# Optimization experiments

Hardware: AMD Instinct MI355X
Metric: run time of the kernel (lower is better)

The kernel has to match this reference:

```python
import jax, jax.numpy as jnp
import numpy as np

MEAN_STOP_TIME_S = 60.0
MIN_ROUTE_LEN = 2
DEMAND_TIME_WEIGHT = 0.5
ROUTE_TIME_WEIGHT = 0.5
UNSERVED_WEIGHT = 5.0

B, N, R, L, K = 64, 512, 40, 20, 4


def setup_inputs() -> dict:
    key = jax.random.key(0)
    ks = jax.random.split(key, 8)
    demand = jax.random.uniform(ks[0], (B, N, N), dtype=jnp.float32) * 10.0
    drive_times = jax.random.uniform(ks[1], (B, N, N), dtype=jnp.float32) * 1800.0
    transit_times = jax.random.uniform(ks[2], (B, N, N), dtype=jnp.float32) * 3600.0
    has_path = jax.random.randint(ks[3], (B, N, N), 0, 2) > 0
    n_transfers = jax.random.randint(ks[4], (B, N, N), 0, 4).astype(jnp.int32)
    # routes with -1 padding past a random per-route length
    routes = jax.random.randint(ks[5], (B, R, L), 0, N).astype(jnp.int32)
    lens = jax.random.randint(ks[6], (B, R), 0, L + 1)
    valid = jnp.arange(L)[None, None, :] < lens[:, :, None]
    batch_routes = jnp.where(valid, routes, -1)
    # per demand-edge route assignments, -1 = unused slot
    route_seqs = (jax.random.randint(ks[7], (B, N, N, K), 0, R + 1) - 1).astype(jnp.int32)
    return {
        'demand': demand, 'drive_times': drive_times, 'transit_times': transit_times,
        'has_path': has_path, 'n_transfers': n_transfers,
        'batch_routes': batch_routes, 'route_seqs': route_seqs,
    }


def _route_leg_times(batch_routes, dtm, mean_stop_time_s):
    # leg (l -> l+1) of each route: dtm[b, from, to] + stop time, masked on valid stops
    frm = batch_routes[:, :, :-1]
    to = batch_routes[:, :, 1:]
    valid = (frm >= 0) & (to >= 0)
    bidx = jnp.arange(dtm.shape[0])[:, None, None]
    times = dtm[bidx, jnp.maximum(frm, 0), jnp.maximum(to, 0)] + mean_stop_time_s
    return jnp.where(valid, times, 0.0)  # [B, R, L-1]


def _per_route_riders(demand, route_seqs, n_routes):
    # segment-sum demand over route ids; -1 slots go to a dump bucket
    def per_b(dem, rs):
        ids = rs.reshape(-1)
        vals = jnp.broadcast_to(dem[..., None], rs.shape).reshape(-1)
        ids = jnp.where(ids < 0, n_routes, ids)
        return jax.ops.segment_sum(vals, ids, num_segments=n_routes + 1)[:n_routes]
    return jax.vmap(per_b)(demand, route_seqs)  # [B, R]


def reference(demand, drive_times, transit_times, has_path, n_transfers,
              batch_routes, route_seqs):
    fdem = demand
    nopath = ~has_path
    route_lens = (batch_routes > -1).sum(-1)  # [B, R]

    n_disconnected = (nopath & (fdem > 0)).sum(axis=(1, 2))
    route_len_delta = jnp.maximum(MIN_ROUTE_LEN - route_lens, 0)
    route_len_delta = jnp.where(route_lens == 0, 0, route_len_delta)
    n_stops_oob = route_len_delta.sum(-1)  # [B]

    nt_eff = jnp.where(nopath, 3, n_transfers)
    tat = jnp.stack([
        (fdem * (nt_eff == 0)).sum(axis=(1, 2)),
        (fdem * (nt_eff == 1)).sum(axis=(1, 2)),
        (fdem * (nt_eff == 2)).sum(axis=(1, 2)),
        (fdem * (nt_eff > 2)).sum(axis=(1, 2)),
    ], axis=-1)  # trips_at_transfers [B, 4]

    trip_times = jnp.where(nopath, 0.0, transit_times)
    total_dmd_time = (fdem * trip_times).sum(axis=(1, 2))
    total_transfers = (fdem * n_transfers.astype(fdem.dtype)).sum(axis=(1, 2))
    unserved = (fdem * nopath).sum(axis=(1, 2))
    total_demand = fdem.sum(axis=(1, 2))

    leg_times = _route_leg_times(batch_routes, drive_times, MEAN_STOP_TIME_S)
    total_route_time = leg_times.sum(axis=(1, 2))
    # symmetric_routes=True: add return-direction legs
    ret = _route_leg_times(batch_routes, jnp.swapaxes(drive_times, 1, 2), MEAN_STOP_TIME_S)
    total_route_time = total_route_time + ret.sum(axis=(1, 2))

    per_route_riders = _per_route_riders(fdem, route_seqs, R)

    # cost assembly
    time_norm = drive_times.max(axis=(1, 2))
    served = total_demand - unserved
    mean_dmd_time = total_dmd_time / (served + 1e-6)
    norm_dmd_time = mean_dmd_time / time_norm
    n_routes_used = (route_lens > 0).sum(-1)
    norm_route_time = total_route_time / (time_norm * n_routes_used + 1e-6)
    n_demand_edges = (fdem > 0).sum(axis=(1, 2))
    frac_uncovered = n_disconnected / n_demand_edges
    denom = n_routes_used * MIN_ROUTE_LEN
    frac_oob = n_stops_oob / (denom + 1e-6)
    cost = (DEMAND_TIME_WEIGHT * norm_dmd_time
            + ROUTE_TIME_WEIGHT * norm_route_time
            + UNSERVED_WEIGHT * (frac_uncovered + frac_oob))
    return cost, per_route_riders, tat, total_route_time


if __name__ == '__main__':
    out = reference(**setup_inputs())
    print([o.shape for o in out])
```

## Files before the change

### kernel.cpp

```cpp
#include <hip/hip_runtime.h>

#define NB 64
#define NDIM 512
#define NNE (NDIM * NDIM)
#define NR 40
#define NL 20
#define SUBS 16
#define IT 16

#define MAIN_STRIDE 256
#define FLAG_OFF (NB * SUBS * MAIN_STRIDE)
#define OUT_RIDERS 64
#define OUT_TAT (64 + NB * NR)
#define OUT_TRT (64 + NB * NR + NB * 4)

__global__ void detect_kernel(const unsigned int* __restrict__ hp, int* __restrict__ flag) {
    unsigned int v = hp[threadIdx.x];
    unsigned long long m = __ballot(v > 1u);
    if (threadIdx.x == 0) *flag = (m != 0ull) ? 1 : 0;
}

struct G {
    float4 dem, tt, dt;
    int4 nt, r0, r1, r2, r3;
    int h0, h1, h2, h3;
};

template<bool BYTE>
__device__ __forceinline__ void ld(G& g,
    const float* __restrict__ pd, const float* __restrict__ pt,
    const float* __restrict__ pdr, const int* __restrict__ pn,
    const void* __restrict__ ph, const int* __restrict__ pr, int o)
{
    g.dem = *(const float4*)(pd + o);
    g.tt  = *(const float4*)(pt + o);
    g.dt  = *(const float4*)(pdr + o);
    g.nt  = *(const int4*)(pn + o);
    g.r0  = *(const int4*)(pr + o * 4);
    g.r1  = *(const int4*)(pr + o * 4 + 4);
    g.r2  = *(const int4*)(pr + o * 4 + 8);
    g.r3  = *(const int4*)(pr + o * 4 + 12);
    if (BYTE) {
        const uchar4 hb = *(const uchar4*)((const unsigned char*)ph + o);
        g.h0 = hb.x; g.h1 = hb.y; g.h2 = hb.z; g.h3 = hb.w;
    } else {
        const int4 hw = *(const int4*)((const int*)ph + o);
        g.h0 = hw.x; g.h1 = hw.y; g.h2 = hw.z; g.h3 = hw.w;
    }
}

__device__ __forceinline__ void procE(float d, float ttv, float dtv, int ntv, int hv,
                                      int i0, int i1, int i2, int i3,
                                      float acc[10], float* __restrict__ bcol)
{
    const bool np_ = (hv == 0);
    const int nte = np_ ? 3 : ntv;
    acc[0] += (nte == 0) ? d : 0.0f;
    acc[1] += (nte == 1) ? d : 0.0f;
    acc[2] += (nte == 2) ? d : 0.0f;
    acc[3] += (nte > 2) ? d : 0.0f;
    acc[4] += np_ ? 0.0f : d * ttv;
    acc[5] += np_ ? d : 0.0f;
    acc[6] += d;
    const bool pos = d > 0.0f;
    acc[7] += (np_ && pos) ? 1.0f : 0.0f;
    acc[8] += pos ? 1.0f : 0.0f;
    acc[9] = fmaxf(acc[9], dtv);

    const unsigned u0 = (unsigned)i0, u1 = (unsigned)i1,
                   u2 = (unsigned)i2, u3 = (unsigned)i3;
    const unsigned b0 = min(u0, (unsigned)(NR - 1));
    const unsigned b1 = min(u1, (unsigned)(NR - 1));
    const unsigned b2 = min(u2, (unsigned)(NR - 1));
    const unsigned b3 = min(u3, (unsigned)(NR - 1));
    const float w0 = (u0 < NR) ? d : 0.0f;
    const float w1 = (u1 < NR) ? d : 0.0f;
    const float w2 = (u2 < NR) ? d : 0.0f;
    const float w3 = (u3 < NR) ? d : 0.0f;
    const float a0 = w0;
    const float a1 = w1 + ((b1 == b0) ? w0 : 0.0f);
    const float a2 = w2 + ((b2 == b0) ? w0 : 0.0f) + ((b2 == b1) ? w1 : 0.0f);
    const float a3 = w3 + ((b3 == b0) ? w0 : 0.0f) + ((b3 == b1) ? w1 : 0.0f)
                        + ((b3 == b2) ? w2 : 0.0f);
    const float v0 = bcol[b0 * 256];
    const float v1 = bcol[b1 * 256];
    const float v2 = bcol[b2 * 256];
    const float v3 = bcol[b3 * 256];
    bcol[b0 * 256] = v0 + a0;
    bcol[b1 * 256] = v1 + a1;
    bcol[b2 * 256] = v2 + a2;
    bcol[b3 * 256] = v3 + a3;
}

__device__ __forceinline__ void procG(const G& g, float acc[10], float* __restrict__ bcol)
{
    procE(g.dem.x, g.tt.x, g.dt.x, g.nt.x, g.h0, g.r0.x, g.r0.y, g.r0.z, g.r0.w, acc, bcol);
    procE(g.dem.y, g.tt.y, g.dt.y, g.nt.y, g.h1, g.r1.x, g.r1.y, g.r1.z, g.r1.w, acc, bcol);
    procE(g.dem.z, g.tt.z, g.dt.z, g.nt.z, g.h2, g.r2.x, g.r2.y, g.r2.z, g.r2.w, acc, bcol);
    procE(g.dem.w, g.tt.w, g.dt.w, g.nt.w, g.h3, g.r3.x, g.r3.y, g.r3.z, g.r3.w, acc, bcol);
}

template<bool BYTE>
__device__ __forceinline__ void mloop(
    const float* __restrict__ pd, const float* __restrict__ pt,
    const float* __restrict__ pdr, const int* __restrict__ pn,
    const void* __restrict__ ph, const int* __restrict__ pr,
    float acc[10], float* __restrict__ bcol)
{
    G A, B;
    ld<BYTE>(A, pd, pt, pdr, pn, ph, pr, 0);
#pragma unroll 1
    for (int it = 0; it < IT - 2; it += 2) {
        ld<BYTE>(B, pd, pt, pdr, pn, ph, pr, (it + 1) * 1024);
        procG(A, acc, bcol);
        ld<BYTE>(A, pd, pt, pdr, pn, ph, pr, (it + 2) * 1024);
        procG(B, acc, bcol);
    }
    ld<BYTE>(B, pd, pt, pdr, pn, ph, pr, (IT - 1) * 1024);
    procG(A, acc, bcol);
    procG(B, acc, bcol);
}

__global__ __launch_bounds__(256, 4) void main_kernel(
    const float* __restrict__ demand,
    const float* __restrict__ transit,
    const float* __restrict__ drive,
    const int* __restrict__ ntr,
    const unsigned char* __restrict__ hp_raw,
    const int* __restrict__ rseq,
    const int* __restrict__ flag,
    float* __restrict__ ws)
{
    __shared__ float bins[NR * 256];
    const int tid = threadIdx.x;
    const int wave = tid >> 6, lane = tid & 63;
    float* __restrict__ bcol = bins + tid;
#pragma unroll
    for (int j = 0; j < NR; ++j) bcol[j * 256] = 0.0f;

    const int b = blockIdx.x >> 4, sub = blockIdx.x & 15;
    const size_t e0 = (size_t)b * NNE + (size_t)sub * (NNE / SUBS) + (size_t)tid * 4;

    float acc[10] = {0, 0, 0, 0, 0, 0, 0, 0, 0, 0};
    if (*flag != 0)
        mloop<true>(demand + e0, transit + e0, drive + e0, ntr + e0,
                    hp_raw + e0, rseq + e0 * 4, acc, bcol);
    else
        mloop<false>(demand + e0, transit + e0, drive + e0, ntr + e0,
                     ((const int*)hp_raw) + e0, rseq + e0 * 4, acc, bcol);

#pragma unroll
    for (int o = 32; o > 0; o >>= 1) {
#pragma unroll
        for (int v = 0; v < 9; ++v) acc[v] += __shfl_down(acc[v], o);
        acc[9] = fmaxf(acc[9], __shfl_down(acc[9], o));
    }
    float* part = ws + (size_t)blockIdx.x * MAIN_STRIDE;
    if (lane == 0) {
#pragma unroll
        for (int v = 0; v < 10; ++v) part[wave * 10 + v] = acc[v];
    }
    __syncthreads();

    if (tid < 4 * NR) {
        const int g = tid / NR, j = tid - g * NR;
        float s = 0.0f;
#pragma unroll 8
        for (int r = g * 64; r < g * 64 + 64; ++r) s += bins[j * 256 + r];
        part[40 + g * NR + j] = s;
    }
}

__global__ __launch_bounds__(64) void final_kernel(
    const float* __restrict__ ws,
    const int* __restrict__ routes,
    const float* __restrict__ drive,
    float* __restrict__ out)
{
    __shared__ float fin[50];
    __shared__ float rt3[3];
    const int b = blockIdx.x;
    const int v = threadIdx.x;

    float t = 0.0f, used = 0.0f, oob = 0.0f;
    if (v < NR) {
        const int* rt = routes + (b * NR + v) * NL;
        int rv[NL];
        int len = 0;
#pragma unroll
        for (int l = 0; l < NL; ++l) { rv[l] = rt[l]; len += (rv[l] > -1) ? 1 : 0; }
        const float* D = drive + (size_t)b * NNE;
#pragma unroll
        for (int l = 0; l < NL - 1; ++l) {
            int f = rv[l], to = rv[l + 1];
            if (f >= 0 && to >= 0)
                t += D[f * NDIM + to] + D[to * NDIM + f] + 120.0f;
        }
        used = (len > 0) ? 1.0f : 0.0f;
        int delta = 2 - len;
        oob = (len > 0 && delta > 0) ? (float)delta : 0.0f;
    }
#pragma unroll
    for (int o = 32; o > 0; o >>= 1) {
        t += __shfl_down(t, o);
        used += __shfl_down(used, o);
        oob += __shfl_down(oob, o);
    }
    if (v == 0) { rt3[0] = t; rt3[1] = used; rt3[2] = oob; }

    const float* base = ws + (size_t)b * SUBS * MAIN_STRIDE;
    if (v < NR) {
        float s = 0.0f;
#pragma unroll 4
        for (int i = 0; i < SUBS * 4; ++i)
            s += base[(i >> 2) * MAIN_STRIDE + 40 + (i & 3) * NR + v];
        fin[v] = s;
    } else if (v < 50) {
        const int k = v - 40;
        if (k == 9) {
            float m = 0.0f;
#pragma unroll 4
            for (int i = 0; i < SUBS * 4; ++i)
                m = fmaxf(m, base[(i >> 2) * MAIN_STRIDE + (i & 3) * 10 + 9]);
            fin[v] = m;
        } else {
            float s = 0.0f;
#pragma unroll 4
            for (int i = 0; i < SUBS * 4; ++i)
                s += base[(i >> 2) * MAIN_STRIDE + (i & 3) * 10 + k];
            fin[v] = s;
        }
    }
    __syncthreads();

    if (v == 0) {
        const float trt = rt3[0], nru = rt3[1], noob = rt3[2];
        const float dmdt = fin[44], uns = fin[45], tdem = fin[46];
        const float ndisc = fin[47], nedge = fin[48], tn = fin[49];
        const float served = tdem - uns;
        const float cost = 0.5f * ((dmdt / (served + 1e-6f)) / tn)
                         + 0.5f * (trt / (tn * nru + 1e-6f))
                         + 5.0f * (ndisc / nedge + noob / (nru * 2.0f + 1e-6f));
        out[b] = cost;
        out[OUT_TRT + b] = trt;
    }
    if (v < NR) out[OUT_RIDERS + b * NR + v] = fin[v];
    if (v >= 40 && v < 44) out[OUT_TAT + b * 4 + (v - 40)] = fin[v];
}

extern "C" void kernel_launch(void* const* d_in, const int* in_sizes, int n_in,
                              void* d_out, int out_size, void* d_ws, size_t ws_size,
                              hipStream_t stream) {
    const float* demand  = (const float*)d_in[0];
    const float* drive   = (const float*)d_in[1];
    const float* transit = (const float*)d_in[2];
    const unsigned char* hp = (const unsigned char*)d_in[3];
    const int* ntr    = (const int*)d_in[4];
    const int* routes = (const int*)d_in[5];
    const int* rseq   = (const int*)d_in[6];
    float* out = (float*)d_out;
    float* ws  = (float*)d_ws;
    int* flag  = (int*)(ws + FLAG_OFF);

    detect_kernel<<<1, 64, 0, stream>>>((const unsigned int*)hp, flag);
    main_kernel<<<NB * SUBS, 256, 0, stream>>>(demand, transit, drive, ntr, hp, rseq, flag, ws);
    final_kernel<<<NB, 64, 0, stream>>>(ws, routes, drive, out);
}
```

Baseline: 140.4 us.

## Use fp16 shared bins, double grid, fold byte-flag detection into main kernel

```diff
diff --git a/kernel.cpp b/kernel.cpp
--- a/kernel.cpp
+++ b/kernel.cpp
@@ -1,57 +1,22 @@
 #include <hip/hip_runtime.h>
+#include <hip/hip_fp16.h>
 
 #define NB 64
 #define NDIM 512
 #define NNE (NDIM * NDIM)
 #define NR 40
 #define NL 20
-#define SUBS 16
-#define IT 16
+#define SUBS 32
+#define IT 8
 
 #define MAIN_STRIDE 256
-#define FLAG_OFF (NB * SUBS * MAIN_STRIDE)
 #define OUT_RIDERS 64
 #define OUT_TAT (64 + NB * NR)
 #define OUT_TRT (64 + NB * NR + NB * 4)
 
-__global__ void detect_kernel(const unsigned int* __restrict__ hp, int* __restrict__ flag) {
-    unsigned int v = hp[threadIdx.x];
-    unsigned long long m = __ballot(v > 1u);
-    if (threadIdx.x == 0) *flag = (m != 0ull) ? 1 : 0;
-}
-
-struct G {
-    float4 dem, tt, dt;
-    int4 nt, r0, r1, r2, r3;
-    int h0, h1, h2, h3;
-};
-
-template<bool BYTE>
-__device__ __forceinline__ void ld(G& g,
-    const float* __restrict__ pd, const float* __restrict__ pt,
-    const float* __restrict__ pdr, const int* __restrict__ pn,
-    const void* __restrict__ ph, const int* __restrict__ pr, int o)
-{
-    g.dem = *(const float4*)(pd + o);
-    g.tt  = *(const float4*)(pt + o);
-    g.dt  = *(const float4*)(pdr + o);
-    g.nt  = *(const int4*)(pn + o);
-    g.r0  = *(const int4*)(pr + o * 4);
-    g.r1  = *(const int4*)(pr + o * 4 + 4);
-    g.r2  = *(const int4*)(pr + o * 4 + 8);
-    g.r3  = *(const int4*)(pr + o * 4 + 12);
-    if (BYTE) {
-        const uchar4 hb = *(const uchar4*)((const unsigned char*)ph + o);
-        g.h0 = hb.x; g.h1 = hb.y; g.h2 = hb.z; g.h3 = hb.w;
-    } else {
-        const int4 hw = *(const int4*)((const int*)ph + o);
-        g.h0 = hw.x; g.h1 = hw.y; g.h2 = hw.z; g.h3 = hw.w;
-    }
-}
-
 __device__ __forceinline__ void procE(float d, float ttv, float dtv, int ntv, int hv,
                                       int i0, int i1, int i2, int i3,
-                                      float acc[10], float* __restrict__ bcol)
+                                      float acc[10], __half* __restrict__ bcol)
 {
     const bool np_ = (hv == 0);
     const int nte = np_ ? 3 : ntv;
@@ -82,22 +47,14 @@
     const float a2 = w2 + ((b2 == b0) ? w0 : 0.0f) + ((b2 == b1) ? w1 : 0.0f);
     const float a3 = w3 + ((b3 == b0) ? w0 : 0.0f) + ((b3 == b1) ? w1 : 0.0f)
                         + ((b3 == b2) ? w2 : 0.0f);
-    const float v0 = bcol[b0 * 256];
-    const float v1 = bcol[b1 * 256];
-    const float v2 = bcol[b2 * 256];
-    const float v3 = bcol[b3 * 256];
-    bcol[b0 * 256] = v0 + a0;
-    bcol[b1 * 256] = v1 + a1;
-    bcol[b2 * 256] = v2 + a2;
-    bcol[b3 * 256] = v3 + a3;
-}
-
-__device__ __forceinline__ void procG(const G& g, float acc[10], float* __restrict__ bcol)
-{
-    procE(g.dem.x, g.tt.x, g.dt.x, g.nt.x, g.h0, g.r0.x, g.r0.y, g.r0.z, g.r0.w, acc, bcol);
-    procE(g.dem.y, g.tt.y, g.dt.y, g.nt.y, g.h1, g.r1.x, g.r1.y, g.r1.z, g.r1.w, acc, bcol);
-    procE(g.dem.z, g.tt.z, g.dt.z, g.nt.z, g.h2, g.r2.x, g.r2.y, g.r2.z, g.r2.w, acc, bcol);
-    procE(g.dem.w, g.tt.w, g.dt.w, g.nt.w, g.h3, g.r3.x, g.r3.y, g.r3.z, g.r3.w, acc, bcol);
+    const float v0 = __half2float(bcol[b0 * 256]);
+    const float v1 = __half2float(bcol[b1 * 256]);
+    const float v2 = __half2float(bcol[b2 * 256]);
+    const float v3 = __half2float(bcol[b3 * 256]);
+    bcol[b0 * 256] = __float2half(v0 + a0);
+    bcol[b1 * 256] = __float2half(v1 + a1);
+    bcol[b2 * 256] = __float2half(v2 + a2);
+    bcol[b3 * 256] = __float2half(v3 + a3);
 }
 
 template<bool BYTE>
@@ -105,44 +62,58 @@
     const float* __restrict__ pd, const float* __restrict__ pt,
     const float* __restrict__ pdr, const int* __restrict__ pn,
     const void* __restrict__ ph, const int* __restrict__ pr,
-    float acc[10], float* __restrict__ bcol)
-{
-    G A, B;
-    ld<BYTE>(A, pd, pt, pdr, pn, ph, pr, 0);
-#pragma unroll 1
-    for (int it = 0; it < IT - 2; it += 2) {
-        ld<BYTE>(B, pd, pt, pdr, pn, ph, pr, (it + 1) * 1024);
-        procG(A, acc, bcol);
-        ld<BYTE>(A, pd, pt, pdr, pn, ph, pr, (it + 2) * 1024);
-        procG(B, acc, bcol);
-    }
-    ld<BYTE>(B, pd, pt, pdr, pn, ph, pr, (IT - 1) * 1024);
-    procG(A, acc, bcol);
-    procG(B, acc, bcol);
-}
-
-__global__ __launch_bounds__(256, 4) void main_kernel(
+    float acc[10], __half* __restrict__ bcol)
+{
+#pragma unroll 2
+    for (int it = 0; it < IT; ++it) {
+        const int o = it * 1024;
+        const float4 dem = *(const float4*)(pd + o);
+        const float4 tt  = *(const float4*)(pt + o);
+        const float4 dt  = *(const float4*)(pdr + o);
+        const int4   nt  = *(const int4*)(pn + o);
+        const int4 r0 = *(const int4*)(pr + o * 4);
+        const int4 r1 = *(const int4*)(pr + o * 4 + 4);
+        const int4 r2 = *(const int4*)(pr + o * 4 + 8);
+        const int4 r3 = *(const int4*)(pr + o * 4 + 12);
+        int h0, h1, h2, h3;
+        if (BYTE) {
+            const uchar4 hb = *(const uchar4*)((const unsigned char*)ph + o);
+            h0 = hb.x; h1 = hb.y; h2 = hb.z; h3 = hb.w;
+        } else {
+            const int4 hw = *(const int4*)((const int*)ph + o);
+            h0 = hw.x; h1 = hw.y; h2 = hw.z; h3 = hw.w;
+        }
+        procE(dem.x, tt.x, dt.x, nt.x, h0, r0.x, r0.y, r0.z, r0.w, acc, bcol);
+        procE(dem.y, tt.y, dt.y, nt.y, h1, r1.x, r1.y, r1.z, r1.w, acc, bcol);
+        procE(dem.z, tt.z, dt.z, nt.z, h2, r2.x, r2.y, r2.z, r2.w, acc, bcol);
+        procE(dem.w, tt.w, dt.w, nt.w, h3, r3.x, r3.y, r3.z, r3.w, acc, bcol);
+    }
+}
+
+__global__ __launch_bounds__(256, 8) void main_kernel(
     const float* __restrict__ demand,
     const float* __restrict__ transit,
     const float* __restrict__ drive,
     const int* __restrict__ ntr,
     const unsigned char* __restrict__ hp_raw,
     const int* __restrict__ rseq,
-    const int* __restrict__ flag,
     float* __restrict__ ws)
 {
-    __shared__ float bins[NR * 256];
+    __shared__ __half bins[NR * 256];
     const int tid = threadIdx.x;
     const int wave = tid >> 6, lane = tid & 63;
-    float* __restrict__ bcol = bins + tid;
-#pragma unroll
-    for (int j = 0; j < NR; ++j) bcol[j * 256] = 0.0f;
-
-    const int b = blockIdx.x >> 4, sub = blockIdx.x & 15;
+    __half* __restrict__ bcol = bins + tid;
+#pragma unroll
+    for (int j = 0; j < NR; ++j) bcol[j * 256] = __float2half(0.0f);
+
+    const unsigned wdet = ((const unsigned*)hp_raw)[tid];
+    const bool isByte = __any(wdet > 1u);
+
+    const int b = blockIdx.x >> 5, sub = blockIdx.x & 31;
     const size_t e0 = (size_t)b * NNE + (size_t)sub * (NNE / SUBS) + (size_t)tid * 4;
 
     float acc[10] = {0, 0, 0, 0, 0, 0, 0, 0, 0, 0};
-    if (*flag != 0)
+    if (isByte)
         mloop<true>(demand + e0, transit + e0, drive + e0, ntr + e0,
                     hp_raw + e0, rseq + e0 * 4, acc, bcol);
     else
@@ -164,9 +135,12 @@
 
     if (tid < 4 * NR) {
         const int g = tid / NR, j = tid - g * NR;
+        const __half* col = bins + j * 256 + g * 64;
+        const int st = (2 * j) & 63;
         float s = 0.0f;
 #pragma unroll 8
-        for (int r = g * 64; r < g * 64 + 64; ++r) s += bins[j * 256 + r];
+        for (int r = 0; r < 64; ++r)
+            s += __half2float(col[(r + st) & 63]);
         part[40 + g * NR + j] = s;
     }
 }
@@ -211,7 +185,6 @@
     const float* base = ws + (size_t)b * SUBS * MAIN_STRIDE;
     if (v < NR) {
         float s = 0.0f;
-#pragma unroll 4
         for (int i = 0; i < SUBS * 4; ++i)
             s += base[(i >> 2) * MAIN_STRIDE + 40 + (i & 3) * NR + v];
         fin[v] = s;
@@ -219,13 +192,11 @@
         const int k = v - 40;
         if (k == 9) {
             float m = 0.0f;
-#pragma unroll 4
             for (int i = 0; i < SUBS * 4; ++i)
                 m = fmaxf(m, base[(i >> 2) * MAIN_STRIDE + (i & 3) * 10 + 9]);
             fin[v] = m;
         } else {
             float s = 0.0f;
-#pragma unroll 4
             for (int i = 0; i < SUBS * 4; ++i)
                 s += base[(i >> 2) * MAIN_STRIDE + (i & 3) * 10 + k];
             fin[v] = s;
@@ -260,9 +231,7 @@
     const int* rseq   = (const int*)d_in[6];
     float* out = (float*)d_out;
     float* ws  = (float*)d_ws;
-    int* flag  = (int*)(ws + FLAG_OFF);
-
-    detect_kernel<<<1, 64, 0, stream>>>((const unsigned int*)hp, flag);
-    main_kernel<<<NB * SUBS, 256, 0, stream>>>(demand, transit, drive, ntr, hp, rseq, flag, ws);
+
+    main_kernel<<<NB * SUBS, 256, 0, stream>>>(demand, transit, drive, ntr, hp, rseq, ws);
     final_kernel<<<NB, 64, 0, stream>>>(ws, routes, drive, out);
 }
```

Result: slower. 175.8 us (+25.2%).
